# Kernel optimization log

Hardware: AMD Instinct MI355X
Metric: run time of the kernel (lower is better)

## Reference

```python
import jax, jax.numpy as jnp
import numpy as np

B, N, E = 8, 5000, 100000
IN_DIM, OUT_DIM = 128, 128
EPS = 1e-5


def setup_inputs() -> dict:
    key = jax.random.key(0)
    ks = jax.random.split(key, 8)
    node_features = jax.random.normal(ks[0], (B, N, IN_DIM), dtype=jnp.float32)
    edge_index = jax.random.randint(ks[1], (B, 2, E), 0, N, dtype=jnp.int32)
    node_mask = jnp.ones((B, N), dtype=jnp.float32)
    edge_mask = jnp.ones((B, E), dtype=jnp.float32)
    s = 1.0 / np.sqrt(IN_DIM)
    W_self = jax.random.uniform(ks[2], (IN_DIM, OUT_DIM), minval=-s, maxval=s, dtype=jnp.float32)
    b_self = jax.random.uniform(ks[3], (OUT_DIM,), minval=-s, maxval=s, dtype=jnp.float32)
    W_nb = jax.random.uniform(ks[4], (IN_DIM, OUT_DIM), minval=-s, maxval=s, dtype=jnp.float32)
    b_nb = jax.random.uniform(ks[5], (OUT_DIM,), minval=-s, maxval=s, dtype=jnp.float32)
    gamma = jnp.ones((OUT_DIM,), dtype=jnp.float32)
    beta = jnp.zeros((OUT_DIM,), dtype=jnp.float32)
    return {"node_features": node_features, "edge_index": edge_index,
            "node_mask": node_mask, "edge_mask": edge_mask,
            "W_self": W_self, "b_self": b_self, "W_nb": W_nb, "b_nb": b_nb,
            "gamma": gamma, "beta": beta}


def _aggregate_mean(x, ei, em):
    # x: [N, D], ei: [2, E], em: [E]. Masked segment-mean over incoming edges.
    src, tgt = ei[0], ei[1]
    sf = x[src] * em[:, None]                                   # [E, D]
    sums = jax.ops.segment_sum(sf, tgt, num_segments=N)         # [N, D]
    cnt = jax.ops.segment_sum(em, tgt, num_segments=N)          # [N]
    return sums / jnp.maximum(cnt, 1.0)[:, None]


def reference(node_features, edge_index, node_mask, edge_mask,
              W_self, b_self, W_nb, b_nb, gamma, beta):
    self_feat = jnp.einsum('bnd,do->bno', node_features, W_self) + b_self
    agg = jax.vmap(_aggregate_mean)(node_features, edge_index, edge_mask)  # [B,N,D]
    nb_feat = jnp.einsum('bnd,do->bno', agg, W_nb) + b_nb
    out = jax.nn.relu(self_feat + nb_feat)
    # dropout in eval mode -> identity
    mu = jnp.mean(out, axis=-1, keepdims=True)
    var = jnp.var(out, axis=-1, keepdims=True)
    out = (out - mu) * jax.lax.rsqrt(var + EPS) * gamma + beta
    return out * node_mask[..., None]
```

## Files before the change

kernel.cpp:

```cpp
#include <hip/hip_runtime.h>


#define B_ 8
#define N_ 5000
#define E_ 100000
#define D_ 128
#define EPS_ 1e-5f
#define NNODES (B_ * N_)
#define NEDGES (B_ * E_)
#define JB 313
#define EPB ((E_ + 255) / 256)
#define FILL_BLOCKS (8 * EPB)
#define CONV_BLOCKS 2500
#define CAP 64
#define LDSP 136

typedef __bf16 bf16x8 __attribute__((ext_vector_type(8)));
typedef float  f32x4  __attribute__((ext_vector_type(4)));

static __device__ __forceinline__ unsigned short f2bf(float f) {
    union { float f; unsigned int i; } c; c.f = f;
    unsigned int i = c.i;
    i += 0x7fffu + ((i >> 16) & 1u);
    return (unsigned short)(i >> 16);
}
static __device__ __forceinline__ float bflo(unsigned int u) {
    return __uint_as_float(u << 16);
}
static __device__ __forceinline__ float bfhi(unsigned int u) {
    return __uint_as_float(u & 0xffff0000u);
}

__global__ __launch_bounds__(256) void fill_k(
    const int* __restrict__ ei, const float* __restrict__ em,
    int* __restrict__ cnt, int2* __restrict__ entries,
    const float* __restrict__ x, unsigned short* __restrict__ xbf,
    const float* __restrict__ Wself, const float* __restrict__ Wnb,
    unsigned short* __restrict__ Bt)
{
    int blk = blockIdx.x;
    if (blk < FILL_BLOCKS) {
        int b = blk & 7;
        int e = (blk >> 3) * 256 + threadIdx.x;
        if (e >= E_) return;
        const int* eib = ei + (size_t)b * 2 * E_;
        int src = eib[e];
        int tgt = eib[E_ + e];
        float m = em[(size_t)b * E_ + e];
        if (m != 0.0f) {
            int g = b * N_ + tgt;
            int slot = atomicAdd(&cnt[g], 1);
            if (slot < CAP)
                entries[((size_t)g << 6) + slot] =
                    make_int2(b * N_ + src, __float_as_int(m));
        }
    } else if (blk < FILL_BLOCKS + CONV_BLOCKS) {
        size_t base = (size_t)(blk - FILL_BLOCKS) * 2048 + threadIdx.x * 8;
        float4 va = *(const float4*)(x + base);
        float4 vb = *(const float4*)(x + base + 4);
        uint4 o;
        o.x = (unsigned int)f2bf(va.x) | ((unsigned int)f2bf(va.y) << 16);
        o.y = (unsigned int)f2bf(va.z) | ((unsigned int)f2bf(va.w) << 16);
        o.z = (unsigned int)f2bf(vb.x) | ((unsigned int)f2bf(vb.y) << 16);
        o.w = (unsigned int)f2bf(vb.z) | ((unsigned int)f2bf(vb.w) << 16);
        *(uint4*)(xbf + base) = o;
    } else {
        int n = blk - FILL_BLOCKS - CONV_BLOCKS;
        int k = threadIdx.x;
        float v = (k < 128) ? Wself[(size_t)k * D_ + n]
                            : Wnb[(size_t)(k - 128) * D_ + n];
        Bt[(size_t)n * 256 + k] = f2bf(v);
    }
}

static __device__ __forceinline__ void gather_node_lds(
    int g, int lane, const unsigned short* __restrict__ xbf,
    const int* __restrict__ cnt, const int2* __restrict__ entries,
    unsigned short* dst)
{
    int dg = cnt[g]; if (dg > CAP) dg = CAP;
    const int2* ep = entries + ((size_t)g << 6);
    int grp = lane >> 4;
    int c8 = lane & 15;

    float a[8];
    #pragma unroll
    for (int i = 0; i < 8; ++i) a[i] = 0.f;
    float cs = 0.f;

    int2 ee = (lane < 16 && lane < dg) ? ep[lane] : make_int2(0, 0);
    int k = 0;
    for (; k + 16 <= dg; k += 16) {
        int2 een = (lane < 16 && k + 16 + lane < dg) ? ep[k + 16 + lane]
                                                     : make_int2(0, 0);
        #pragma unroll
        for (int j = 0; j < 4; ++j) {
            int eidx = 4 * j + grp;
            int   sj = __shfl(ee.x, eidx, 64);
            float mj = __int_as_float(__shfl(ee.y, eidx, 64));
            uint4 v = *(const uint4*)(xbf + (size_t)sj * D_ + 8 * c8);
            a[0] += bflo(v.x) * mj; a[1] += bfhi(v.x) * mj;
            a[2] += bflo(v.y) * mj; a[3] += bfhi(v.y) * mj;
            a[4] += bflo(v.z) * mj; a[5] += bfhi(v.z) * mj;
            a[6] += bflo(v.w) * mj; a[7] += bfhi(v.w) * mj;
            cs += mj;
        }
        ee = een;
    }
    int rem = dg - k;
    if (rem > 0) {
        #pragma unroll
        for (int j = 0; j < 4; ++j) {
            int eidx = 4 * j + grp;
            int   sj = __shfl(ee.x, eidx, 64);
            float mj = __int_as_float(__shfl(ee.y, eidx, 64));
            if (eidx < rem) {
                uint4 v = *(const uint4*)(xbf + (size_t)sj * D_ + 8 * c8);
                a[0] += bflo(v.x) * mj; a[1] += bfhi(v.x) * mj;
                a[2] += bflo(v.y) * mj; a[3] += bfhi(v.y) * mj;
                a[4] += bflo(v.z) * mj; a[5] += bfhi(v.z) * mj;
                a[6] += bflo(v.w) * mj; a[7] += bfhi(v.w) * mj;
                cs += mj;
            }
        }
    }

    #pragma unroll
    for (int i = 0; i < 8; ++i) {
        a[i] += __shfl_xor(a[i], 16, 64);
        a[i] += __shfl_xor(a[i], 32, 64);
    }
    cs += __shfl_xor(cs, 16, 64);
    cs += __shfl_xor(cs, 32, 64);

    if (lane < 16) {
        float inv = 1.0f / fmaxf(cs, 1.0f);
        uint4 o;
        o.x = (unsigned int)f2bf(a[0] * inv) | ((unsigned int)f2bf(a[1] * inv) << 16);
        o.y = (unsigned int)f2bf(a[2] * inv) | ((unsigned int)f2bf(a[3] * inv) << 16);
        o.z = (unsigned int)f2bf(a[4] * inv) | ((unsigned int)f2bf(a[5] * inv) << 16);
        o.w = (unsigned int)f2bf(a[6] * inv) | ((unsigned int)f2bf(a[7] * inv) << 16);
        *(uint4*)(dst + 8 * c8) = o;
    }
}

__global__ __launch_bounds__(256) void fused_k(
    const unsigned short* __restrict__ xbf, const int* __restrict__ cnt,
    const int2* __restrict__ entries,
    const unsigned short* __restrict__ Bt,
    const float* __restrict__ bself, const float* __restrict__ bnb,
    const float* __restrict__ gamma, const float* __restrict__ beta,
    const float* __restrict__ nmask, float* __restrict__ out)
{
    __shared__ unsigned short xs[16][LDSP];
    __shared__ unsigned short as[16][LDSP];
    __shared__ float red[4][2][16];

    int t = threadIdx.x;
    int lane = t & 63, wv = t >> 6;
    int b = blockIdx.x & 7;
    int j = blockIdx.x >> 3;
    int i0 = j * 16;
    int limit = N_ - i0; if (limit > 16) limit = 16;

    #pragma unroll
    for (int lr = wv * 4; lr < wv * 4 + 4; ++lr) {
        unsigned int v = 0;
        if (lr < limit) {
            int g = b * N_ + i0 + lr;
            v = ((const unsigned int*)(xbf + (size_t)g * D_))[lane];
        }
        ((unsigned int*)&xs[lr][0])[lane] = v;
    }
    for (int lr = wv * 4; lr < wv * 4 + 4; ++lr) {
        if (lr < limit) {
            gather_node_lds(b * N_ + i0 + lr, lane, xbf, cnt, entries, &as[lr][0]);
        } else if (lane < 16) {
            *(uint4*)&as[lr][8 * (lane & 15)] = make_uint4(0u, 0u, 0u, 0u);
        }
    }
    __syncthreads();

    int quad = lane >> 4;
    int lcol = lane & 15;

    f32x4 acc[2];
    acc[0] = (f32x4)0.0f;
    acc[1] = (f32x4)0.0f;

    #pragma unroll
    for (int kk = 0; kk < 4; ++kk) {
        int kof = kk * 32 + quad * 8;
        bf16x8 a = *(const bf16x8*)&xs[lcol][kof];
        #pragma unroll
        for (int p = 0; p < 2; ++p) {
            int tt = wv * 2 + p;
            bf16x8 bf = *(const bf16x8*)(Bt + (size_t)(tt * 16 + lcol) * 256 + kof);
            acc[p] = __builtin_amdgcn_mfma_f32_16x16x32_bf16(a, bf, acc[p], 0, 0, 0);
        }
    }
    #pragma unroll
    for (int kk = 0; kk < 4; ++kk) {
        int kof = kk * 32 + quad * 8;
        bf16x8 a = *(const bf16x8*)&as[lcol][kof];
        #pragma unroll
        for (int p = 0; p < 2; ++p) {
            int tt = wv * 2 + p;
            bf16x8 bf = *(const bf16x8*)(Bt + (size_t)(tt * 16 + lcol) * 256 + 128 + kof);
            acc[p] = __builtin_amdgcn_mfma_f32_16x16x32_bf16(a, bf, acc[p], 0, 0, 0);
        }
    }

    float h[2][4];
    float s[4] = {0, 0, 0, 0}, q[4] = {0, 0, 0, 0};
    float gam[2], bet[2];
    #pragma unroll
    for (int p = 0; p < 2; ++p) {
        int col = (wv * 2 + p) * 16 + lcol;
        float bs = bself[col] + bnb[col];
        gam[p] = gamma[col];
        bet[p] = beta[col];
        #pragma unroll
        for (int r = 0; r < 4; ++r) {
            float v = fmaxf(acc[p][r] + bs, 0.0f);
            h[p][r] = v;
            s[r] += v;
            q[r] += v * v;
        }
    }
    #pragma unroll
    for (int r = 0; r < 4; ++r) {
        #pragma unroll
        for (int off = 1; off <= 8; off <<= 1) {
            s[r] += __shfl_xor(s[r], off, 64);
            q[r] += __shfl_xor(q[r], off, 64);
        }
    }
    if (lcol == 0) {
        #pragma unroll
        for (int r = 0; r < 4; ++r) {
            red[wv][0][quad * 4 + r] = s[r];
            red[wv][1][quad * 4 + r] = q[r];
        }
    }
    __syncthreads();

    #pragma unroll
    for (int r = 0; r < 4; ++r) {
        int row = quad * 4 + r;
        int irow = i0 + row;
        if (irow >= N_) continue;
        float S = red[0][0][row] + red[1][0][row] + red[2][0][row] + red[3][0][row];
        float Q = red[0][1][row] + red[1][1][row] + red[2][1][row] + red[3][1][row];
        float mu = S * (1.0f / D_);
        float var = Q * (1.0f / D_) - mu * mu;
        float rin = rsqrtf(fmaxf(var, 0.0f) + EPS_);
        int g = b * N_ + irow;
        float mk = nmask[g];
        float* op = out + (size_t)g * D_;
        #pragma unroll
        for (int p = 0; p < 2; ++p) {
            int col = (wv * 2 + p) * 16 + lcol;
            op[col] = ((h[p][r] - mu) * rin * gam[p] + bet[p]) * mk;
        }
    }
}

extern "C" void kernel_launch(void* const* d_in, const int* in_sizes, int n_in,
                              void* d_out, int out_size, void* d_ws, size_t ws_size,
                              hipStream_t stream)
{
    const float* x     = (const float*)d_in[0];
    const int*   ei    = (const int*)d_in[1];
    const float* nmask = (const float*)d_in[2];
    const float* em    = (const float*)d_in[3];
    const float* Wself = (const float*)d_in[4];
    const float* bself = (const float*)d_in[5];
    const float* Wnb   = (const float*)d_in[6];
    const float* bnb   = (const float*)d_in[7];
    const float* gamma = (const float*)d_in[8];
    const float* beta  = (const float*)d_in[9];
    float* out = (float*)d_out;

    int* cnt = (int*)d_ws;
    int2* entries = (int2*)(cnt + NNODES);
    unsigned short* Bt = (unsigned short*)(entries + (size_t)NNODES * CAP);
    unsigned short* xbf = Bt + (size_t)128 * 256;

    hipMemsetAsync(cnt, 0, NNODES * sizeof(int), stream);
    fill_k<<<FILL_BLOCKS + CONV_BLOCKS + 128, 256, 0, stream>>>(
        ei, em, cnt, entries, x, xbf, Wself, Wnb, Bt);
    fused_k<<<8 * JB, 256, 0, stream>>>(xbf, cnt, entries, Bt,
                                        bself, bnb, gamma, beta, nmask, out);
}
```

Measured before the change: 174.4 us.

## Load-balance neighbor gather across block via shared edge list and LDS atomics

The per-node gather, where each wave handled four nodes and looped over their edges, is replaced by a block-level scheme. The edge entries of all 16 nodes are compacted into a shared list with prefix offsets. The four waves then take edges round-robin and accumulate into fp32 shared buffers with LDS atomicAdd, and the result is converted to bf16 afterwards. The aim is to remove load imbalance across waves from uneven degrees, at the cost of serial prefix work on one thread, extra barriers, LDS atomic contention and smaller 4-byte-per-lane gathers.

```diff
diff --git a/kernel.cpp b/kernel.cpp
--- a/kernel.cpp
+++ b/kernel.cpp
@@ -73,77 +73,6 @@
     }
 }
 
-static __device__ __forceinline__ void gather_node_lds(
-    int g, int lane, const unsigned short* __restrict__ xbf,
-    const int* __restrict__ cnt, const int2* __restrict__ entries,
-    unsigned short* dst)
-{
-    int dg = cnt[g]; if (dg > CAP) dg = CAP;
-    const int2* ep = entries + ((size_t)g << 6);
-    int grp = lane >> 4;
-    int c8 = lane & 15;
-
-    float a[8];
-    #pragma unroll
-    for (int i = 0; i < 8; ++i) a[i] = 0.f;
-    float cs = 0.f;
-
-    int2 ee = (lane < 16 && lane < dg) ? ep[lane] : make_int2(0, 0);
-    int k = 0;
-    for (; k + 16 <= dg; k += 16) {
-        int2 een = (lane < 16 && k + 16 + lane < dg) ? ep[k + 16 + lane]
-                                                     : make_int2(0, 0);
-        #pragma unroll
-        for (int j = 0; j < 4; ++j) {
-            int eidx = 4 * j + grp;
-            int   sj = __shfl(ee.x, eidx, 64);
-            float mj = __int_as_float(__shfl(ee.y, eidx, 64));
-            uint4 v = *(const uint4*)(xbf + (size_t)sj * D_ + 8 * c8);
-            a[0] += bflo(v.x) * mj; a[1] += bfhi(v.x) * mj;
-            a[2] += bflo(v.y) * mj; a[3] += bfhi(v.y) * mj;
-            a[4] += bflo(v.z) * mj; a[5] += bfhi(v.z) * mj;
-            a[6] += bflo(v.w) * mj; a[7] += bfhi(v.w) * mj;
-            cs += mj;
-        }
-        ee = een;
-    }
-    int rem = dg - k;
-    if (rem > 0) {
-        #pragma unroll
-        for (int j = 0; j < 4; ++j) {
-            int eidx = 4 * j + grp;
-            int   sj = __shfl(ee.x, eidx, 64);
-            float mj = __int_as_float(__shfl(ee.y, eidx, 64));
-            if (eidx < rem) {
-                uint4 v = *(const uint4*)(xbf + (size_t)sj * D_ + 8 * c8);
-                a[0] += bflo(v.x) * mj; a[1] += bfhi(v.x) * mj;
-                a[2] += bflo(v.y) * mj; a[3] += bfhi(v.y) * mj;
-                a[4] += bflo(v.z) * mj; a[5] += bfhi(v.z) * mj;
-                a[6] += bflo(v.w) * mj; a[7] += bfhi(v.w) * mj;
-                cs += mj;
-            }
-        }
-    }
-
-    #pragma unroll
-    for (int i = 0; i < 8; ++i) {
-        a[i] += __shfl_xor(a[i], 16, 64);
-        a[i] += __shfl_xor(a[i], 32, 64);
-    }
-    cs += __shfl_xor(cs, 16, 64);
-    cs += __shfl_xor(cs, 32, 64);
-
-    if (lane < 16) {
-        float inv = 1.0f / fmaxf(cs, 1.0f);
-        uint4 o;
-        o.x = (unsigned int)f2bf(a[0] * inv) | ((unsigned int)f2bf(a[1] * inv) << 16);
-        o.y = (unsigned int)f2bf(a[2] * inv) | ((unsigned int)f2bf(a[3] * inv) << 16);
-        o.z = (unsigned int)f2bf(a[4] * inv) | ((unsigned int)f2bf(a[5] * inv) << 16);
-        o.w = (unsigned int)f2bf(a[6] * inv) | ((unsigned int)f2bf(a[7] * inv) << 16);
-        *(uint4*)(dst + 8 * c8) = o;
-    }
-}
-
 __global__ __launch_bounds__(256) void fused_k(
     const unsigned short* __restrict__ xbf, const int* __restrict__ cnt,
     const int2* __restrict__ entries,
@@ -154,6 +83,11 @@
 {
     __shared__ unsigned short xs[16][LDSP];
     __shared__ unsigned short as[16][LDSP];
+    __shared__ float aggf[16][128];
+    __shared__ float csumf[16];
+    __shared__ int   csh[16];
+    __shared__ int   pre[17];
+    __shared__ int2  list[16 * CAP];
     __shared__ float red[4][2][16];
 
     int t = threadIdx.x;
@@ -161,23 +95,73 @@
     int b = blockIdx.x & 7;
     int j = blockIdx.x >> 3;
     int i0 = j * 16;
+    int g0 = b * N_ + i0;
     int limit = N_ - i0; if (limit > 16) limit = 16;
 
     #pragma unroll
     for (int lr = wv * 4; lr < wv * 4 + 4; ++lr) {
         unsigned int v = 0;
-        if (lr < limit) {
-            int g = b * N_ + i0 + lr;
-            v = ((const unsigned int*)(xbf + (size_t)g * D_))[lane];
-        }
+        if (lr < limit)
+            v = ((const unsigned int*)(xbf + (size_t)(g0 + lr) * D_))[lane];
         ((unsigned int*)&xs[lr][0])[lane] = v;
     }
-    for (int lr = wv * 4; lr < wv * 4 + 4; ++lr) {
-        if (lr < limit) {
-            gather_node_lds(b * N_ + i0 + lr, lane, xbf, cnt, entries, &as[lr][0]);
-        } else if (lane < 16) {
-            *(uint4*)&as[lr][8 * (lane & 15)] = make_uint4(0u, 0u, 0u, 0u);
-        }
+    {
+        float* az = &aggf[0][0];
+        #pragma unroll
+        for (int i = t; i < 16 * 128; i += 256) az[i] = 0.0f;
+        if (t < 16) csumf[t] = 0.0f;
+    }
+    if (t == 0) {
+        int r = 0;
+        #pragma unroll
+        for (int jj = 0; jj < 16; ++jj) {
+            int c = (jj < limit) ? cnt[g0 + jj] : 0;
+            if (c > CAP) c = CAP;
+            csh[jj] = c;
+            pre[jj] = r;
+            r += c;
+        }
+        pre[16] = r;
+    }
+    __syncthreads();
+
+    for (int s = t; s < 16 * CAP; s += 256) {
+        int jj = s >> 6, k = s & 63;
+        if (k < csh[jj]) {
+            int2 e = entries[((size_t)(g0 + jj) << 6) + k];
+            list[pre[jj] + k] = make_int2((e.x & 0xFFFFF) | (jj << 20), e.y);
+        }
+    }
+    __syncthreads();
+
+    {
+        int tot = pre[16];
+        for (int i = wv; i < tot; i += 4) {
+            int2 e = list[i];
+            int   src = e.x & 0xFFFFF;
+            int   jj  = ((unsigned)e.x) >> 20;
+            float m   = __int_as_float(e.y);
+            unsigned int v = ((const unsigned int*)(xbf + (size_t)src * D_))[lane];
+            atomicAdd(&aggf[jj][lane],      bflo(v) * m);
+            atomicAdd(&aggf[jj][64 + lane], bfhi(v) * m);
+            if (lane == 0) atomicAdd(&csumf[jj], m);
+        }
+    }
+    __syncthreads();
+
+    {
+        int jj = t >> 4, c = t & 15;
+        float inv = 1.0f / fmaxf(csumf[jj], 1.0f);
+        uint4 o;
+        float lo0 = aggf[jj][4 * c + 0] * inv, hi0 = aggf[jj][64 + 4 * c + 0] * inv;
+        float lo1 = aggf[jj][4 * c + 1] * inv, hi1 = aggf[jj][64 + 4 * c + 1] * inv;
+        float lo2 = aggf[jj][4 * c + 2] * inv, hi2 = aggf[jj][64 + 4 * c + 2] * inv;
+        float lo3 = aggf[jj][4 * c + 3] * inv, hi3 = aggf[jj][64 + 4 * c + 3] * inv;
+        o.x = (unsigned int)f2bf(lo0) | ((unsigned int)f2bf(hi0) << 16);
+        o.y = (unsigned int)f2bf(lo1) | ((unsigned int)f2bf(hi1) << 16);
+        o.z = (unsigned int)f2bf(lo2) | ((unsigned int)f2bf(hi2) << 16);
+        o.w = (unsigned int)f2bf(lo3) | ((unsigned int)f2bf(hi3) << 16);
+        *(uint4*)&as[jj][8 * c] = o;
     }
     __syncthreads();
 
```

Result: slower. 685.6 us (+293.1%).

## Split neighbor gather into separate kernel writing bf16 aggregate buffer

Applied to the files above, without the earlier changes.

The gather-mean over incoming edges moves out of the fused GEMM+LayerNorm kernel into its own kernel, one wave per node across 10000 blocks, writing a bf16 aggregate to workspace. The GEMM kernel then just loads the x and aggregate rows into LDS. The aim is more parallelism and latency hiding for the irregular gather, since before each wave walked four nodes in sequence and the GEMM blocks stalled on it. In exchange it adds a kernel launch and a round trip of the aggregate buffer through global memory.

```diff
diff --git a/kernel.cpp b/kernel.cpp
--- a/kernel.cpp
+++ b/kernel.cpp
@@ -73,11 +73,15 @@
     }
 }
 
-static __device__ __forceinline__ void gather_node_lds(
-    int g, int lane, const unsigned short* __restrict__ xbf,
-    const int* __restrict__ cnt, const int2* __restrict__ entries,
-    unsigned short* dst)
-{
+__global__ __launch_bounds__(256) void gather_k(
+    const unsigned short* __restrict__ xbf, const int* __restrict__ cnt,
+    const int2* __restrict__ entries, unsigned short* __restrict__ agg)
+{
+    int wv = threadIdx.x >> 6, lane = threadIdx.x & 63;
+    int b = blockIdx.x & 7;
+    int i = (blockIdx.x >> 3) * 4 + wv;
+    int g = b * N_ + i;
+
     int dg = cnt[g]; if (dg > CAP) dg = CAP;
     const int2* ep = entries + ((size_t)g << 6);
     int grp = lane >> 4;
@@ -85,7 +89,7 @@
 
     float a[8];
     #pragma unroll
-    for (int i = 0; i < 8; ++i) a[i] = 0.f;
+    for (int k = 0; k < 8; ++k) a[k] = 0.f;
     float cs = 0.f;
 
     int2 ee = (lane < 16 && lane < dg) ? ep[lane] : make_int2(0, 0);
@@ -126,9 +130,9 @@
     }
 
     #pragma unroll
-    for (int i = 0; i < 8; ++i) {
-        a[i] += __shfl_xor(a[i], 16, 64);
-        a[i] += __shfl_xor(a[i], 32, 64);
+    for (int q = 0; q < 8; ++q) {
+        a[q] += __shfl_xor(a[q], 16, 64);
+        a[q] += __shfl_xor(a[q], 32, 64);
     }
     cs += __shfl_xor(cs, 16, 64);
     cs += __shfl_xor(cs, 32, 64);
@@ -140,13 +144,12 @@
         o.y = (unsigned int)f2bf(a[2] * inv) | ((unsigned int)f2bf(a[3] * inv) << 16);
         o.z = (unsigned int)f2bf(a[4] * inv) | ((unsigned int)f2bf(a[5] * inv) << 16);
         o.w = (unsigned int)f2bf(a[6] * inv) | ((unsigned int)f2bf(a[7] * inv) << 16);
-        *(uint4*)(dst + 8 * c8) = o;
-    }
-}
-
-__global__ __launch_bounds__(256) void fused_k(
-    const unsigned short* __restrict__ xbf, const int* __restrict__ cnt,
-    const int2* __restrict__ entries,
+        *(uint4*)(agg + (size_t)g * D_ + 8 * c8) = o;
+    }
+}
+
+__global__ __launch_bounds__(256) void gemm_ln_k(
+    const unsigned short* __restrict__ xbf, const unsigned short* __restrict__ agg,
     const unsigned short* __restrict__ Bt,
     const float* __restrict__ bself, const float* __restrict__ bnb,
     const float* __restrict__ gamma, const float* __restrict__ beta,
@@ -161,23 +164,18 @@
     int b = blockIdx.x & 7;
     int j = blockIdx.x >> 3;
     int i0 = j * 16;
+    int g0 = b * N_ + i0;
     int limit = N_ - i0; if (limit > 16) limit = 16;
 
     #pragma unroll
     for (int lr = wv * 4; lr < wv * 4 + 4; ++lr) {
-        unsigned int v = 0;
+        unsigned int vx = 0, va = 0;
         if (lr < limit) {
-            int g = b * N_ + i0 + lr;
-            v = ((const unsigned int*)(xbf + (size_t)g * D_))[lane];
-        }
-        ((unsigned int*)&xs[lr][0])[lane] = v;
-    }
-    for (int lr = wv * 4; lr < wv * 4 + 4; ++lr) {
-        if (lr < limit) {
-            gather_node_lds(b * N_ + i0 + lr, lane, xbf, cnt, entries, &as[lr][0]);
-        } else if (lane < 16) {
-            *(uint4*)&as[lr][8 * (lane & 15)] = make_uint4(0u, 0u, 0u, 0u);
-        }
+            vx = ((const unsigned int*)(xbf + (size_t)(g0 + lr) * D_))[lane];
+            va = ((const unsigned int*)(agg + (size_t)(g0 + lr) * D_))[lane];
+        }
+        ((unsigned int*)&xs[lr][0])[lane] = vx;
+        ((unsigned int*)&as[lr][0])[lane] = va;
     }
     __syncthreads();
 
@@ -286,10 +284,12 @@
     int2* entries = (int2*)(cnt + NNODES);
     unsigned short* Bt = (unsigned short*)(entries + (size_t)NNODES * CAP);
     unsigned short* xbf = Bt + (size_t)128 * 256;
+    unsigned short* agg = xbf + (size_t)NNODES * D_;
 
     hipMemsetAsync(cnt, 0, NNODES * sizeof(int), stream);
     fill_k<<<FILL_BLOCKS + CONV_BLOCKS + 128, 256, 0, stream>>>(
         ei, em, cnt, entries, x, xbf, Wself, Wnb, Bt);
-    fused_k<<<8 * JB, 256, 0, stream>>>(xbf, cnt, entries, Bt,
-                                        bself, bnb, gamma, beta, nmask, out);
-}
+    gather_k<<<1250 * 8, 256, 0, stream>>>(xbf, cnt, entries, agg);
+    gemm_ln_k<<<8 * JB, 256, 0, stream>>>(xbf, agg, Bt,
+                                          bself, bnb, gamma, beta, nmask, out);
+}
```

New measurement: 173.4 us. Within noise of the previous version (-0.6%).

## Pack edge entries into 32-bit words and process two edges per thread

Applied to the files above, without the earlier changes.

Each adjacency entry now packs the global source node index (low 16 bits) and the edge mask as bf16 (high 16 bits) into one 32-bit word instead of an int2. This halves the scattered entry writes in the fill kernel and the entry reads plus shuffles in the gather. The fill phase also handles two edges per thread with vectorized int2/float2 loads, which reduces block count and load instructions. The trade-off is that the mask is rounded to bf16 and source indices must fit in 16 bits, which holds since B*N is under 65536.

```diff
diff --git a/kernel.cpp b/kernel.cpp
--- a/kernel.cpp
+++ b/kernel.cpp
@@ -9,8 +9,8 @@
 #define NNODES (B_ * N_)
 #define NEDGES (B_ * E_)
 #define JB 313
-#define EPB ((E_ + 255) / 256)
-#define FILL_BLOCKS (8 * EPB)
+#define PPB ((E_ / 2 + 255) / 256)
+#define FILL_BLOCKS (8 * PPB)
 #define CONV_BLOCKS 2500
 #define CAP 64
 #define LDSP 136
@@ -33,7 +33,7 @@
 
 __global__ __launch_bounds__(256) void fill_k(
     const int* __restrict__ ei, const float* __restrict__ em,
-    int* __restrict__ cnt, int2* __restrict__ entries,
+    int* __restrict__ cnt, unsigned int* __restrict__ entries,
     const float* __restrict__ x, unsigned short* __restrict__ xbf,
     const float* __restrict__ Wself, const float* __restrict__ Wnb,
     unsigned short* __restrict__ Bt)
@@ -41,18 +41,27 @@
     int blk = blockIdx.x;
     if (blk < FILL_BLOCKS) {
         int b = blk & 7;
-        int e = (blk >> 3) * 256 + threadIdx.x;
-        if (e >= E_) return;
+        int p = (blk >> 3) * 256 + threadIdx.x;
+        if (p >= E_ / 2) return;
+        int e = 2 * p;
         const int* eib = ei + (size_t)b * 2 * E_;
-        int src = eib[e];
-        int tgt = eib[E_ + e];
-        float m = em[(size_t)b * E_ + e];
-        if (m != 0.0f) {
-            int g = b * N_ + tgt;
+        int2   sv = *(const int2*)(eib + e);
+        int2   tv = *(const int2*)(eib + E_ + e);
+        float2 mv = *(const float2*)(em + (size_t)b * E_ + e);
+        int gb = b * N_;
+        if (mv.x != 0.0f) {
+            int g = gb + tv.x;
             int slot = atomicAdd(&cnt[g], 1);
             if (slot < CAP)
                 entries[((size_t)g << 6) + slot] =
-                    make_int2(b * N_ + src, __float_as_int(m));
+                    (unsigned int)(gb + sv.x) | ((unsigned int)f2bf(mv.x) << 16);
+        }
+        if (mv.y != 0.0f) {
+            int g = gb + tv.y;
+            int slot = atomicAdd(&cnt[g], 1);
+            if (slot < CAP)
+                entries[((size_t)g << 6) + slot] =
+                    (unsigned int)(gb + sv.y) | ((unsigned int)f2bf(mv.y) << 16);
         }
     } else if (blk < FILL_BLOCKS + CONV_BLOCKS) {
         size_t base = (size_t)(blk - FILL_BLOCKS) * 2048 + threadIdx.x * 8;
@@ -75,11 +84,11 @@
 
 static __device__ __forceinline__ void gather_node_lds(
     int g, int lane, const unsigned short* __restrict__ xbf,
-    const int* __restrict__ cnt, const int2* __restrict__ entries,
+    const int* __restrict__ cnt, const unsigned int* __restrict__ entries,
     unsigned short* dst)
 {
     int dg = cnt[g]; if (dg > CAP) dg = CAP;
-    const int2* ep = entries + ((size_t)g << 6);
+    const unsigned int* ep = entries + ((size_t)g << 6);
     int grp = lane >> 4;
     int c8 = lane & 15;
 
@@ -88,16 +97,15 @@
     for (int i = 0; i < 8; ++i) a[i] = 0.f;
     float cs = 0.f;
 
-    int2 ee = (lane < 16 && lane < dg) ? ep[lane] : make_int2(0, 0);
+    unsigned int ee = (lane < 16 && lane < dg) ? ep[lane] : 0u;
     int k = 0;
     for (; k + 16 <= dg; k += 16) {
-        int2 een = (lane < 16 && k + 16 + lane < dg) ? ep[k + 16 + lane]
-                                                     : make_int2(0, 0);
+        unsigned int een = (lane < 16 && k + 16 + lane < dg) ? ep[k + 16 + lane] : 0u;
         #pragma unroll
         for (int j = 0; j < 4; ++j) {
-            int eidx = 4 * j + grp;
-            int   sj = __shfl(ee.x, eidx, 64);
-            float mj = __int_as_float(__shfl(ee.y, eidx, 64));
+            unsigned int ej = (unsigned int)__shfl((int)ee, 4 * j + grp, 64);
+            int   sj = ej & 0xFFFFu;
+            float mj = __uint_as_float(ej & 0xFFFF0000u);
             uint4 v = *(const uint4*)(xbf + (size_t)sj * D_ + 8 * c8);
             a[0] += bflo(v.x) * mj; a[1] += bfhi(v.x) * mj;
             a[2] += bflo(v.y) * mj; a[3] += bfhi(v.y) * mj;
@@ -112,8 +120,9 @@
         #pragma unroll
         for (int j = 0; j < 4; ++j) {
             int eidx = 4 * j + grp;
-            int   sj = __shfl(ee.x, eidx, 64);
-            float mj = __int_as_float(__shfl(ee.y, eidx, 64));
+            unsigned int ej = (unsigned int)__shfl((int)ee, eidx, 64);
+            int   sj = ej & 0xFFFFu;
+            float mj = __uint_as_float(ej & 0xFFFF0000u);
             if (eidx < rem) {
                 uint4 v = *(const uint4*)(xbf + (size_t)sj * D_ + 8 * c8);
                 a[0] += bflo(v.x) * mj; a[1] += bfhi(v.x) * mj;
@@ -126,9 +135,9 @@
     }
 
     #pragma unroll
-    for (int i = 0; i < 8; ++i) {
-        a[i] += __shfl_xor(a[i], 16, 64);
-        a[i] += __shfl_xor(a[i], 32, 64);
+    for (int q = 0; q < 8; ++q) {
+        a[q] += __shfl_xor(a[q], 16, 64);
+        a[q] += __shfl_xor(a[q], 32, 64);
     }
     cs += __shfl_xor(cs, 16, 64);
     cs += __shfl_xor(cs, 32, 64);
@@ -146,7 +155,7 @@
 
 __global__ __launch_bounds__(256) void fused_k(
     const unsigned short* __restrict__ xbf, const int* __restrict__ cnt,
-    const int2* __restrict__ entries,
+    const unsigned int* __restrict__ entries,
     const unsigned short* __restrict__ Bt,
     const float* __restrict__ bself, const float* __restrict__ bnb,
     const float* __restrict__ gamma, const float* __restrict__ beta,
@@ -161,20 +170,19 @@
     int b = blockIdx.x & 7;
     int j = blockIdx.x >> 3;
     int i0 = j * 16;
+    int g0 = b * N_ + i0;
     int limit = N_ - i0; if (limit > 16) limit = 16;
 
     #pragma unroll
     for (int lr = wv * 4; lr < wv * 4 + 4; ++lr) {
         unsigned int v = 0;
-        if (lr < limit) {
-            int g = b * N_ + i0 + lr;
-            v = ((const unsigned int*)(xbf + (size_t)g * D_))[lane];
-        }
+        if (lr < limit)
+            v = ((const unsigned int*)(xbf + (size_t)(g0 + lr) * D_))[lane];
         ((unsigned int*)&xs[lr][0])[lane] = v;
     }
     for (int lr = wv * 4; lr < wv * 4 + 4; ++lr) {
         if (lr < limit) {
-            gather_node_lds(b * N_ + i0 + lr, lane, xbf, cnt, entries, &as[lr][0]);
+            gather_node_lds(g0 + lr, lane, xbf, cnt, entries, &as[lr][0]);
         } else if (lane < 16) {
             *(uint4*)&as[lr][8 * (lane & 15)] = make_uint4(0u, 0u, 0u, 0u);
         }
@@ -283,7 +291,7 @@
     float* out = (float*)d_out;
 
     int* cnt = (int*)d_ws;
-    int2* entries = (int2*)(cnt + NNODES);
+    unsigned int* entries = (unsigned int*)(cnt + NNODES);
     unsigned short* Bt = (unsigned short*)(entries + (size_t)NNODES * CAP);
     unsigned short* xbf = Bt + (size_t)128 * 256;
 
```

After: 167.0 us. -4.2%, faster.
